# Performance work log

Hardware: AMD Instinct MI355X
Metric: run time of the kernel (lower is better)

The kernel has to match this reference:

```python
import jax, jax.numpy as jnp
import numpy as np

B = 2048
D = 128
N_ENTITY = 100000

def setup_inputs() -> dict:
    key = jax.random.key(0)
    k1, k2, k3 = jax.random.split(key, 3)
    entity_embeddings = jax.random.normal(k1, (B, D), dtype=jnp.float32)
    entity_embs = jax.random.normal(k2, (N_ENTITY, D), dtype=jnp.float32)
    rec_entity_bias = jnp.zeros((N_ENTITY,), dtype=jnp.float32)  # nn.Parameter(torch.zeros(n_entity))
    y = jax.random.randint(k3, (B,), 0, N_ENTITY, dtype=jnp.int64)
    return {"entity_embeddings": entity_embeddings, "entity_embs": entity_embs,
            "rec_entity_bias": rec_entity_bias, "y": y}

def reference(entity_embeddings, entity_embs, rec_entity_bias, y):
    # entities_score = F.linear(entity_embeddings, entity_embs, bias)  -> [B, n_entity]
    logits = jnp.einsum('bd,nd->bn', entity_embeddings, entity_embs) + rec_entity_bias
    # CrossEntropyLoss (mean reduction): -log_softmax(logits)[b, y_b]
    logp = jax.nn.log_softmax(logits, axis=-1)
    nll = -jnp.take_along_axis(logp, y[:, None], axis=-1)[:, 0]
    return jnp.mean(nll)
```

## Files before the change

kernel.cpp:

```cpp
#include <hip/hip_runtime.h>
#include <stdint.h>

#define B_BATCH 2048
#define D_K     128
#define N_ENT   100000
#define TROWS   64
#define NTILES  ((N_ENT + TROWS - 1) / TROWS)
#define N_PAD   (NTILES * TROWS)
#define ESPLIT  128
#define NCG     16
#define LOG2E_F 1.4426950408889634f

#if __has_builtin(__builtin_amdgcn_exp2f)
#define FEXP2(x) __builtin_amdgcn_exp2f(x)
#else
#define FEXP2(x) exp2f(x)
#endif

typedef __attribute__((ext_vector_type(8))) __bf16 bf16x8;
typedef __attribute__((ext_vector_type(8))) short  short8;
typedef __attribute__((ext_vector_type(4))) float  f32x4;

__device__ __forceinline__ short f2bf(float x) {
  unsigned int u = __float_as_uint(x);
  unsigned int r = (u + 0x7fffu + ((u >> 16) & 1u)) >> 16;
  return (short)r;
}

__device__ __forceinline__ short8 pack8(f32x4 a, f32x4 b) {
  short8 v;
  v[0] = f2bf(a[0]); v[1] = f2bf(a[1]); v[2] = f2bf(a[2]); v[3] = f2bf(a[3]);
  v[4] = f2bf(b[0]); v[5] = f2bf(b[1]); v[6] = f2bf(b[2]); v[7] = f2bf(b[3]);
  return v;
}

__global__ __launch_bounds__(256)
void prep_kernel(const float* __restrict__ X, const float* __restrict__ E,
                 const float* __restrict__ bias, const int* __restrict__ y,
                 unsigned short* __restrict__ Xb, unsigned short* __restrict__ Eb,
                 float* __restrict__ biasL, float* __restrict__ S,
                 float* __restrict__ tdot)
{
  int tid = blockIdx.x * 256 + threadIdx.x;
  if (Eb) {
    int row = tid >> 4, s = tid & 15;
    f32x4 f0 = {0.f,0.f,0.f,0.f}, f1 = {0.f,0.f,0.f,0.f};
    if (row < N_ENT) {
      const float* src = E + (size_t)row * D_K + s * 8;
      f0 = *(const f32x4*)src;
      f1 = *(const f32x4*)(src + 4);
    }
    int sg = s ^ (row & 7);
    *(short8*)(Eb + (size_t)row * D_K + sg * 8) = pack8(f0, f1);
  }
  if (tid < B_BATCH * D_K / 8) {
    int i = tid * 8;
    f32x4 a = *(const f32x4*)(X + i), b = *(const f32x4*)(X + i + 4);
    *(short8*)(Xb + i) = pack8(a, b);
  }
  if (tid < B_BATCH * 16) {
    int b = tid >> 4, sl = tid & 15;
    int yb = y[b];
    const float* xr = X + (size_t)b  * D_K + sl * 8;
    const float* er = E + (size_t)yb * D_K + sl * 8;
    f32x4 a0 = *(const f32x4*)xr,      a1 = *(const f32x4*)(xr + 4);
    f32x4 e0 = *(const f32x4*)er,      e1 = *(const f32x4*)(er + 4);
    float d = a0[0]*e0[0] + a0[1]*e0[1] + a0[2]*e0[2] + a0[3]*e0[3]
            + a1[0]*e1[0] + a1[1]*e1[1] + a1[2]*e1[2] + a1[3]*e1[3];
    #pragma unroll
    for (int sh = 1; sh <= 8; sh <<= 1) d += __shfl_xor(d, sh);
    if (sl == 0) tdot[b] = d + bias[yb];
  }
  if (tid < N_PAD) biasL[tid] = (tid < N_ENT) ? bias[tid] * LOG2E_F : -1e30f;
  if (tid < B_BATCH) S[tid] = 0.f;
}

template<bool PRE>
__global__ __launch_bounds__(256, 4)
void fused_kernel(const unsigned short* __restrict__ Xb,
                  const unsigned short* __restrict__ Eb,
                  const float* __restrict__ Ef,
                  const float* __restrict__ biasL,
                  float* __restrict__ S)
{
  __shared__ __align__(16) unsigned short tile[2][TROWS * D_K];

  const int bid    = blockIdx.x;
  const int stripe = (bid & 7) * 16 + (bid >> 7);
  const int cg     = (bid >> 3) & 15;
  const int t    = threadIdx.x;
  const int lane = t & 63;
  const int w    = t >> 6;
  const int lg   = lane >> 4;
  const int l15  = lane & 15;
  const int col0 = cg * 128 + w * 32;

  bf16x8 Breg[2][4];
  #pragma unroll
  for (int nj = 0; nj < 2; ++nj)
    #pragma unroll
    for (int kk = 0; kk < 4; ++kk)
      Breg[nj][kk] = __builtin_bit_cast(bf16x8,
          *(const short8*)(Xb + (size_t)(col0 + nj * 16 + l15) * D_K
                              + kk * 32 + lg * 8));

  float rs[2] = {0.f, 0.f};

  auto STAGE = [&](int buf, int g) {
    #pragma unroll
    for (int i = 0; i < 4; ++i) {
      const unsigned short* gp =
          Eb + ((size_t)g * TROWS + w * 16 + i * 4) * D_K + lane * 8;
      unsigned short* lp = &tile[buf][(w * 16 + i * 4) * D_K];
      __builtin_amdgcn_global_load_lds(
          (const __attribute__((address_space(1))) void*)gp,
          (__attribute__((address_space(3))) void*)lp, 16, 0, 0);
    }
  };

  f32x4 R[8];
  auto GLOAD = [&](int g) {
    #pragma unroll
    for (int i = 0; i < 4; ++i) {
      int gr = g * TROWS + w * 16 + i * 4 + lg;
      f32x4 z = {0.f,0.f,0.f,0.f};
      R[2*i] = z; R[2*i+1] = z;
      if (gr < N_ENT) {
        const float* src = Ef + (size_t)gr * D_K + l15 * 8;
        R[2*i]   = *(const f32x4*)src;
        R[2*i+1] = *(const f32x4*)(src + 4);
      }
    }
  };
  auto WRITE = [&](int buf) {
    #pragma unroll
    for (int i = 0; i < 4; ++i) {
      int rl = w * 16 + i * 4 + lg;
      int off = rl * D_K + ((l15 * 8) ^ ((rl & 7) << 3));
      *(short8*)&tile[buf][off] = pack8(R[2*i], R[2*i+1]);
    }
  };

  int cur = 0;
  if (PRE) STAGE(0, stripe); else GLOAD(stripe);

  for (int g = stripe; g < NTILES; g += ESPLIT) {
    const int gn = g + ESPLIT;
    if (PRE) {
      __syncthreads();
      if (gn < NTILES) STAGE(cur ^ 1, gn);
    } else {
      WRITE(cur);
      if (gn < NTILES) GLOAD(gn);
      __syncthreads();
    }

    const float* blp = biasL + g * TROWS;
    #pragma unroll
    for (int c = 0; c < 4; ++c) {
      f32x4 bl = *(const f32x4*)(blp + c * 16 + lg * 4);
      bf16x8 A[4];
      #pragma unroll
      for (int kk = 0; kk < 4; ++kk) {
        int off = (c * 16 + l15) * D_K + (((kk * 32) + lg * 8) ^ ((l15 & 7) << 3));
        A[kk] = __builtin_bit_cast(bf16x8, *(const short8*)&tile[cur][off]);
      }
      f32x4 a0 = {0.f,0.f,0.f,0.f}, a1 = {0.f,0.f,0.f,0.f};
      #pragma unroll
      for (int kk = 0; kk < 4; ++kk) {
        a0 = __builtin_amdgcn_mfma_f32_16x16x32_bf16(A[kk], Breg[0][kk], a0, 0, 0, 0);
        a1 = __builtin_amdgcn_mfma_f32_16x16x32_bf16(A[kk], Breg[1][kk], a1, 0, 0, 0);
      }
      float e0 = FEXP2(fmaf(a0[0], LOG2E_F, bl[0]));
      float e1 = FEXP2(fmaf(a0[1], LOG2E_F, bl[1]));
      float e2 = FEXP2(fmaf(a0[2], LOG2E_F, bl[2]));
      float e3 = FEXP2(fmaf(a0[3], LOG2E_F, bl[3]));
      rs[0] += (e0 + e1) + (e2 + e3);
      float f0 = FEXP2(fmaf(a1[0], LOG2E_F, bl[0]));
      float f1 = FEXP2(fmaf(a1[1], LOG2E_F, bl[1]));
      float f2 = FEXP2(fmaf(a1[2], LOG2E_F, bl[2]));
      float f3 = FEXP2(fmaf(a1[3], LOG2E_F, bl[3]));
      rs[1] += (f0 + f1) + (f2 + f3);
    }
    cur ^= 1;
  }

  #pragma unroll
  for (int nj = 0; nj < 2; ++nj) {
    float s = rs[nj];
    s += __shfl_xor(s, 16);
    s += __shfl_xor(s, 32);
    if (lane < 16) atomicAdd(&S[col0 + nj * 16 + lane], s);
  }
}

__global__ __launch_bounds__(256)
void final_kernel(const float* __restrict__ S, const float* __restrict__ tdot,
                  float* __restrict__ out)
{
  __shared__ float wsum[4];
  int t = threadIdx.x;
  float acc = 0.f;
  #pragma unroll
  for (int j = 0; j < B_BATCH / 256; ++j) {
    int b = j * 256 + t;
    acc += 0.6931471805599453f * log2f(S[b]) - tdot[b];
  }
  #pragma unroll
  for (int sh = 1; sh <= 32; sh <<= 1) acc += __shfl_xor(acc, sh);
  if ((t & 63) == 0) wsum[t >> 6] = acc;
  __syncthreads();
  if (t == 0) out[0] = (wsum[0] + wsum[1] + wsum[2] + wsum[3]) / (float)B_BATCH;
}

extern "C" void kernel_launch(void* const* d_in, const int* in_sizes, int n_in,
                              void* d_out, int out_size, void* d_ws, size_t ws_size,
                              hipStream_t stream)
{
  (void)in_sizes; (void)n_in; (void)out_size;
  const float* X    = (const float*)d_in[0];
  const float* E    = (const float*)d_in[1];
  const float* bias = (const float*)d_in[2];
  const int*   y    = (const int*)d_in[3];
  float* out = (float*)d_out;

  char* p = (char*)d_ws;
  float*          Sacc  = (float*)p;                 p += (size_t)B_BATCH * 4;
  float*          tdot  = (float*)p;                 p += (size_t)B_BATCH * 4;
  unsigned short* Xb    = (unsigned short*)p;        p += (size_t)B_BATCH * D_K * 2;
  float*          biasL = (float*)p;                 p += (size_t)N_PAD * 4;
  unsigned short* Eb    = (unsigned short*)p;        p += (size_t)N_PAD * D_K * 2;
  const size_t need = (size_t)(p - (char*)d_ws);
  const bool pre = ws_size >= need;

  prep_kernel<<<N_PAD * 16 / 256, 256, 0, stream>>>(X, E, bias, y, Xb,
                                                    pre ? Eb : nullptr,
                                                    biasL, Sacc, tdot);
  if (pre)
    fused_kernel<true><<<ESPLIT * NCG, 256, 0, stream>>>(Xb, Eb, E, biasL, Sacc);
  else
    fused_kernel<false><<<ESPLIT * NCG, 256, 0, stream>>>(Xb, Eb, E, biasL, Sacc);
  final_kernel<<<1, 256, 0, stream>>>(Sacc, tdot, out);
}
```

Before: 155.6 us.

## Widen per-wave batch tile to 64 columns and truncate bf16 conversion of E

Each block now covers 256 batch columns (64 per wave, four MFMA accumulators per wave) instead of 128, which halves the number of column groups. Every entity tile staged into LDS is therefore reused across twice as many batch rows, halving the re-reads of the bf16 entity matrix. The prep kernel also converts E to bf16 by plain truncation with byte-permute instead of round-to-nearest, which cuts ALU work but adds a small precision bias. The wider tile raises register pressure (16 B fragments held in registers) and halves the grid size.

```diff
diff --git a/kernel.cpp b/kernel.cpp
--- a/kernel.cpp
+++ b/kernel.cpp
@@ -8,7 +8,7 @@
 #define NTILES  ((N_ENT + TROWS - 1) / TROWS)
 #define N_PAD   (NTILES * TROWS)
 #define ESPLIT  128
-#define NCG     16
+#define NCG     8
 #define LOG2E_F 1.4426950408889634f
 
 #if __has_builtin(__builtin_amdgcn_exp2f)
@@ -20,6 +20,7 @@
 typedef __attribute__((ext_vector_type(8))) __bf16 bf16x8;
 typedef __attribute__((ext_vector_type(8))) short  short8;
 typedef __attribute__((ext_vector_type(4))) float  f32x4;
+typedef __attribute__((ext_vector_type(4))) unsigned int u32x4;
 
 __device__ __forceinline__ short f2bf(float x) {
   unsigned int u = __float_as_uint(x);
@@ -32,6 +33,15 @@
   v[0] = f2bf(a[0]); v[1] = f2bf(a[1]); v[2] = f2bf(a[2]); v[3] = f2bf(a[3]);
   v[4] = f2bf(b[0]); v[5] = f2bf(b[1]); v[6] = f2bf(b[2]); v[7] = f2bf(b[3]);
   return v;
+}
+
+__device__ __forceinline__ short8 pack8t(f32x4 a, f32x4 b) {
+  u32x4 w;
+  w[0] = __builtin_amdgcn_perm(__float_as_uint(a[1]), __float_as_uint(a[0]), 0x07060302u);
+  w[1] = __builtin_amdgcn_perm(__float_as_uint(a[3]), __float_as_uint(a[2]), 0x07060302u);
+  w[2] = __builtin_amdgcn_perm(__float_as_uint(b[1]), __float_as_uint(b[0]), 0x07060302u);
+  w[3] = __builtin_amdgcn_perm(__float_as_uint(b[3]), __float_as_uint(b[2]), 0x07060302u);
+  return __builtin_bit_cast(short8, w);
 }
 
 __global__ __launch_bounds__(256)
@@ -51,7 +61,7 @@
       f1 = *(const f32x4*)(src + 4);
     }
     int sg = s ^ (row & 7);
-    *(short8*)(Eb + (size_t)row * D_K + sg * 8) = pack8(f0, f1);
+    *(short8*)(Eb + (size_t)row * D_K + sg * 8) = pack8t(f0, f1);
   }
   if (tid < B_BATCH * D_K / 8) {
     int i = tid * 8;
@@ -86,25 +96,25 @@
   __shared__ __align__(16) unsigned short tile[2][TROWS * D_K];
 
   const int bid    = blockIdx.x;
-  const int stripe = (bid & 7) * 16 + (bid >> 7);
-  const int cg     = (bid >> 3) & 15;
+  const int stripe = (bid & 7) * 16 + (bid >> 6);
+  const int cg     = (bid >> 3) & 7;
   const int t    = threadIdx.x;
   const int lane = t & 63;
   const int w    = t >> 6;
   const int lg   = lane >> 4;
   const int l15  = lane & 15;
-  const int col0 = cg * 128 + w * 32;
-
-  bf16x8 Breg[2][4];
-  #pragma unroll
-  for (int nj = 0; nj < 2; ++nj)
+  const int col0 = cg * 256 + w * 64;
+
+  bf16x8 Breg[4][4];
+  #pragma unroll
+  for (int nj = 0; nj < 4; ++nj)
     #pragma unroll
     for (int kk = 0; kk < 4; ++kk)
       Breg[nj][kk] = __builtin_bit_cast(bf16x8,
           *(const short8*)(Xb + (size_t)(col0 + nj * 16 + l15) * D_K
                               + kk * 32 + lg * 8));
 
-  float rs[2] = {0.f, 0.f};
+  float rs[4] = {0.f, 0.f, 0.f, 0.f};
 
   auto STAGE = [&](int buf, int g) {
     #pragma unroll
@@ -165,28 +175,29 @@
         int off = (c * 16 + l15) * D_K + (((kk * 32) + lg * 8) ^ ((l15 & 7) << 3));
         A[kk] = __builtin_bit_cast(bf16x8, *(const short8*)&tile[cur][off]);
       }
-      f32x4 a0 = {0.f,0.f,0.f,0.f}, a1 = {0.f,0.f,0.f,0.f};
-      #pragma unroll
-      for (int kk = 0; kk < 4; ++kk) {
-        a0 = __builtin_amdgcn_mfma_f32_16x16x32_bf16(A[kk], Breg[0][kk], a0, 0, 0, 0);
-        a1 = __builtin_amdgcn_mfma_f32_16x16x32_bf16(A[kk], Breg[1][kk], a1, 0, 0, 0);
+      f32x4 acc[4];
+      #pragma unroll
+      for (int nj = 0; nj < 4; ++nj) acc[nj] = (f32x4){0.f, 0.f, 0.f, 0.f};
+      #pragma unroll
+      for (int kk = 0; kk < 4; ++kk)
+        #pragma unroll
+        for (int nj = 0; nj < 4; ++nj)
+          acc[nj] = __builtin_amdgcn_mfma_f32_16x16x32_bf16(
+              A[kk], Breg[nj][kk], acc[nj], 0, 0, 0);
+      #pragma unroll
+      for (int nj = 0; nj < 4; ++nj) {
+        float e0 = FEXP2(fmaf(acc[nj][0], LOG2E_F, bl[0]));
+        float e1 = FEXP2(fmaf(acc[nj][1], LOG2E_F, bl[1]));
+        float e2 = FEXP2(fmaf(acc[nj][2], LOG2E_F, bl[2]));
+        float e3 = FEXP2(fmaf(acc[nj][3], LOG2E_F, bl[3]));
+        rs[nj] += (e0 + e1) + (e2 + e3);
       }
-      float e0 = FEXP2(fmaf(a0[0], LOG2E_F, bl[0]));
-      float e1 = FEXP2(fmaf(a0[1], LOG2E_F, bl[1]));
-      float e2 = FEXP2(fmaf(a0[2], LOG2E_F, bl[2]));
-      float e3 = FEXP2(fmaf(a0[3], LOG2E_F, bl[3]));
-      rs[0] += (e0 + e1) + (e2 + e3);
-      float f0 = FEXP2(fmaf(a1[0], LOG2E_F, bl[0]));
-      float f1 = FEXP2(fmaf(a1[1], LOG2E_F, bl[1]));
-      float f2 = FEXP2(fmaf(a1[2], LOG2E_F, bl[2]));
-      float f3 = FEXP2(fmaf(a1[3], LOG2E_F, bl[3]));
-      rs[1] += (f0 + f1) + (f2 + f3);
     }
     cur ^= 1;
   }
 
   #pragma unroll
-  for (int nj = 0; nj < 2; ++nj) {
+  for (int nj = 0; nj < 4; ++nj) {
     float s = rs[nj];
     s += __shfl_xor(s, 16);
     s += __shfl_xor(s, 32);
```

Result: slower. 227.4 us (+46.1%).
